# Performance work log

Hardware: AMD Instinct MI355X
Metric: run time of the kernel (lower is better)

Reference implementation:

```python
import jax, jax.numpy as jnp
import numpy as np

B, LATENT, HIDDEN, HEAD_H, OUT = 262144, 64, 512, 64, 4
EPS = 1e-5


def _layernorm(a, g, b):
    mu = jnp.mean(a, axis=-1, keepdims=True)
    var = jnp.mean(jnp.square(a - mu), axis=-1, keepdims=True)
    return (a - mu) / jnp.sqrt(var + EPS) * g + b


def _leaky(a):
    return jnp.where(a >= 0, a, 0.2 * a)


def setup_inputs() -> dict:
    key = jax.random.key(0)
    ks = jax.random.split(key, 12)
    s = lambda fan_in: 1.0 / np.sqrt(fan_in)
    return {
        "z": jax.random.normal(ks[0], (B, LATENT), dtype=jnp.float32),
        "x": jax.random.randint(ks[1], (B,), 0, 2, dtype=jnp.int32),
        "y": jax.random.randint(ks[2], (B,), 0, 2, dtype=jnp.int32),
        # encoder params (Linear stored as [in, out])
        "W1": jax.random.normal(ks[3], (LATENT, HIDDEN), dtype=jnp.float32) * s(LATENT),
        "b1": jnp.zeros((HIDDEN,), dtype=jnp.float32),
        "g1": jnp.ones((HIDDEN,), dtype=jnp.float32),
        "beta1": jnp.zeros((HIDDEN,), dtype=jnp.float32),
        "W2": jax.random.normal(ks[4], (HIDDEN, HIDDEN), dtype=jnp.float32) * s(HIDDEN),
        "b2": jnp.zeros((HIDDEN,), dtype=jnp.float32),
        "g2": jnp.ones((HIDDEN,), dtype=jnp.float32),
        "beta2": jnp.zeros((HIDDEN,), dtype=jnp.float32),
        # 4 setting-specific heads, stacked on leading axis k = 2*x + y
        "Wh1": jax.random.normal(ks[5], (4, HIDDEN, HEAD_H), dtype=jnp.float32) * s(HIDDEN),
        "bh1": jnp.zeros((4, HEAD_H), dtype=jnp.float32),
        "Wh2": jax.random.normal(ks[6], (4, HEAD_H, OUT), dtype=jnp.float32) * s(HEAD_H),
        "bh2": jnp.zeros((4, OUT), dtype=jnp.float32),
    }


def reference(z, x, y, W1, b1, g1, beta1, W2, b2, g2, beta2, Wh1, bh1, Wh2, bh2):
    # encoder: Linear -> LayerNorm -> LeakyReLU(0.2), twice
    h = _leaky(_layernorm(z @ W1 + b1, g1, beta1))          # [B, HIDDEN]
    h = _leaky(_layernorm(h @ W2 + b2, g2, beta2))          # [B, HIDDEN]
    # all 4 heads in one pass, then per-row select (equivalent to mask routing)
    t = jax.nn.relu(jnp.einsum("bh,khd->bkd", h, Wh1) + bh1)  # [B, 4, HEAD_H]
    logits_all = jnp.einsum("bkd,kdo->bko", t, Wh2) + bh2     # [B, 4, OUT]
    k = 2 * x + y                                              # head index per row
    logits = logits_all[jnp.arange(logits_all.shape[0]), k]    # [B, OUT]
    return jax.nn.softmax(logits, axis=-1)
```

## Files before the change

kernel.cpp:

```cpp
#include <hip/hip_runtime.h>

#define MT 48
#define TS 520
#define NROWS 262144
#define EPSV 1e-5f

typedef __attribute__((ext_vector_type(8))) short short8;
typedef __attribute__((ext_vector_type(4))) float floatx4;
typedef __attribute__((ext_vector_type(2))) float floatx2;
typedef __attribute__((ext_vector_type(4))) unsigned int uintx4;
typedef __attribute__((ext_vector_type(2))) unsigned int uintx2;

__device__ __forceinline__ unsigned short f2bf(float f) {
    unsigned u = __builtin_bit_cast(unsigned, f);
    u += 0x7fff + ((u >> 16) & 1);
    return (unsigned short)(u >> 16);
}
__device__ __forceinline__ float bf2f(short s) {
    unsigned u = ((unsigned)(unsigned short)s) << 16;
    return __builtin_bit_cast(float, u);
}
__device__ __forceinline__ unsigned cvtpk(float a, float b) {
    unsigned r;
    asm("v_cvt_pk_bf16_f32 %0, %1, %2" : "=v"(r) : "v"(a), "v"(b));
    return r;
}
template<int C>
__device__ __forceinline__ float dpp_add(float v) {
    int t = __builtin_amdgcn_update_dpp(0, __builtin_bit_cast(int, v), C, 0xf, 0xf, true);
    return v + __builtin_bit_cast(float, t);
}
__device__ __forceinline__ float red16(float v) {
    v = dpp_add<0x111>(v);
    v = dpp_add<0x112>(v);
    v = dpp_add<0x114>(v);
    v = dpp_add<0x118>(v);
    return v;
}

__global__ void convert_weights(const float* __restrict__ W1, const float* __restrict__ W2,
                                const float* __restrict__ Wh1, short* __restrict__ ws) {
    int idx = blockIdx.x * 256 + threadIdx.x;
    if (idx < 32768) {
        int j = idx & 7, lane = (idx >> 3) & 63, c = idx >> 9;
        int ks = c & 1, nt = (c >> 1) & 7, w = c >> 4;
        int k = ks * 32 + (lane >> 4) * 8 + j;
        int n = w * 128 + nt * 16 + (lane & 15);
        ws[idx] = (short)f2bf(W1[k * 512 + n]);
    } else if (idx < 32768 + 262144) {
        int jdx = idx - 32768;
        int j = jdx & 7, lane = (jdx >> 3) & 63, c = jdx >> 9;
        int nt = c & 7, ks = (c >> 3) & 15, w = c >> 7;
        int kp = ks * 32 + (lane >> 4) * 8 + j;
        int k  = (kp & 0x180) + ((kp & 7) << 4) + ((kp >> 3) & 15);
        int n = w * 128 + nt * 16 + (lane & 15);
        ws[idx] = (short)f2bf(W2[k * 512 + n]);
    } else if (idx < 32768 + 262144 + 131072) {
        int jdx = idx - (32768 + 262144);
        int j = jdx & 7, lane = (jdx >> 3) & 63, c = jdx >> 9;
        int nt = c & 3, ks = (c >> 2) & 15, w = c >> 6;
        int kp = ks * 32 + (lane >> 4) * 8 + j;
        int k  = (kp & 0x180) + ((kp & 7) << 4) + ((kp >> 3) & 15);
        int col = w * 64 + nt * 16 + (lane & 15);
        int kk = col >> 6, d = col & 63;
        ws[idx] = (short)f2bf(Wh1[(kk * 512 + k) * 64 + d]);
    }
}

__global__ __launch_bounds__(256, 2) void fused_kernel(
    const float* __restrict__ z, const int* __restrict__ x, const int* __restrict__ y,
    const float* __restrict__ b1, const float* __restrict__ g1, const float* __restrict__ be1,
    const float* __restrict__ b2, const float* __restrict__ g2, const float* __restrict__ be2,
    const float* __restrict__ bh1, const float* __restrict__ Wh2, const float* __restrict__ bh2,
    const short* __restrict__ ws, float* __restrict__ out)
{
    __shared__ __align__(16) short tile[MT * TS];
    __shared__ float pstats[MT][8];
    __shared__ floatx2 rstats[MT];

    int tid  = threadIdx.x;
    int wave = tid >> 6;
    int lane = tid & 63;
    int quad = lane >> 4;
    int l16  = lane & 15;
    int blk0 = blockIdx.x * MT;
    int nslab = wave * 128;

    const short* bbase1 = ws + wave * (16 * 512) + lane * 8;
    const short* bbase2 = ws + 32768 + wave * (16 * 8 * 512) + lane * 8;
    const short* bbase3 = ws + 32768 + 262144 + wave * (16 * 4 * 512) + lane * 8;

    floatx4 acc[3][8];

#pragma unroll
    for (int mt = 0; mt < 3; mt++)
#pragma unroll
        for (int nt = 0; nt < 8; nt++) acc[mt][nt] = (floatx4){0.f, 0.f, 0.f, 0.f};

    __builtin_amdgcn_s_setprio(1);
#pragma unroll
    for (int ks = 0; ks < 2; ks++) {
        short8 afr[3];
#pragma unroll
        for (int mt = 0; mt < 3; mt++) {
            int row = blk0 + mt * 16 + l16;
            row = (row < NROWS) ? row : (NROWS - 1);
            const float* zp = z + row * 64 + ks * 32 + quad * 8;
            floatx4 f0 = *(const floatx4*)zp;
            floatx4 f1 = *(const floatx4*)(zp + 4);
            uintx4 up;
            up[0] = cvtpk(f0[0], f0[1]); up[1] = cvtpk(f0[2], f0[3]);
            up[2] = cvtpk(f1[0], f1[1]); up[3] = cvtpk(f1[2], f1[3]);
            afr[mt] = __builtin_bit_cast(short8, up);
        }
#pragma unroll
        for (int nt = 0; nt < 8; nt++) {
            short8 b = *(const short8*)(bbase1 + (nt * 2 + ks) * 512);
#pragma unroll
            for (int mt = 0; mt < 3; mt++)
                acc[mt][nt] = __builtin_amdgcn_mfma_f32_16x16x32_bf16(afr[mt], b, acc[mt][nt], 0, 0, 0);
        }
    }
    __builtin_amdgcn_s_setprio(0);

    {
#pragma unroll
        for (int nt = 0; nt < 8; nt++) {
            float bv = b1[nslab + nt * 16 + l16];
#pragma unroll
            for (int mt = 0; mt < 3; mt++)
#pragma unroll
                for (int r2 = 0; r2 < 4; r2++) acc[mt][nt][r2] += bv;
        }
        float sum[3][4] = {}, sq[3][4] = {};
#pragma unroll
        for (int mt = 0; mt < 3; mt++)
#pragma unroll
            for (int nt = 0; nt < 8; nt++)
#pragma unroll
                for (int r2 = 0; r2 < 4; r2++) {
                    float v = acc[mt][nt][r2];
                    sum[mt][r2] += v; sq[mt][r2] += v * v;
                }
#pragma unroll
        for (int mt = 0; mt < 3; mt++)
#pragma unroll
            for (int r2 = 0; r2 < 4; r2++) {
                sum[mt][r2] = red16(sum[mt][r2]);
                sq[mt][r2]  = red16(sq[mt][r2]);
            }
        if (l16 == 15) {
#pragma unroll
            for (int mt = 0; mt < 3; mt++)
#pragma unroll
                for (int r2 = 0; r2 < 4; r2++) {
                    int row = mt * 16 + quad * 4 + r2;
                    *(floatx2*)&pstats[row][wave * 2] = (floatx2){sum[mt][r2], sq[mt][r2]};
                }
        }
    }
    __syncthreads();
    if (tid < MT) {
        float s = pstats[tid][0] + pstats[tid][2] + pstats[tid][4] + pstats[tid][6];
        float q = pstats[tid][1] + pstats[tid][3] + pstats[tid][5] + pstats[tid][7];
        float mean = s * (1.f / 512.f);
        float var  = q * (1.f / 512.f) - mean * mean;
        rstats[tid] = (floatx2){mean, rsqrtf(var + EPSV)};
    }
    __syncthreads();
    {
        floatx2 st[3][4];
#pragma unroll
        for (int mt = 0; mt < 3; mt++)
#pragma unroll
            for (int r2 = 0; r2 < 4; r2++) st[mt][r2] = rstats[mt * 16 + quad * 4 + r2];
        float gv[8], bev[8];
#pragma unroll
        for (int nt = 0; nt < 8; nt++) {
            int col = nslab + nt * 16 + l16;
            gv[nt] = g1[col]; bev[nt] = be1[col];
        }
#pragma unroll
        for (int mt = 0; mt < 3; mt++)
#pragma unroll
            for (int r2 = 0; r2 < 4; r2++) {
                int row = mt * 16 + quad * 4 + r2;
                float mean = st[mt][r2][0], rstd = st[mt][r2][1];
                float f[8];
#pragma unroll
                for (int nt = 0; nt < 8; nt++) {
                    float v = (acc[mt][nt][r2] - mean) * rstd * gv[nt] + bev[nt];
                    f[nt] = fmaxf(v, 0.2f * v);
                }
                uintx4 up;
                up[0] = cvtpk(f[0], f[1]); up[1] = cvtpk(f[2], f[3]);
                up[2] = cvtpk(f[4], f[5]); up[3] = cvtpk(f[6], f[7]);
                *(uintx4*)&tile[row * TS + nslab + l16 * 8] = up;
            }
    }
    __syncthreads();

#pragma unroll
    for (int mt = 0; mt < 3; mt++)
#pragma unroll
        for (int nt = 0; nt < 8; nt++) acc[mt][nt] = (floatx4){0.f, 0.f, 0.f, 0.f};

    __builtin_amdgcn_s_setprio(1);
    for (int ks = 0; ks < 16; ks++) {
        short8 afr[3];
#pragma unroll
        for (int mt = 0; mt < 3; mt++) {
            int row = mt * 16 + l16;
            afr[mt] = *(const short8*)&tile[row * TS + ks * 32 + quad * 8];
        }
#pragma unroll
        for (int nt = 0; nt < 8; nt++) {
            short8 b = *(const short8*)(bbase2 + (ks * 8 + nt) * 512);
#pragma unroll
            for (int mt = 0; mt < 3; mt++)
                acc[mt][nt] = __builtin_amdgcn_mfma_f32_16x16x32_bf16(afr[mt], b, acc[mt][nt], 0, 0, 0);
        }
    }
    __builtin_amdgcn_s_setprio(0);
    {
#pragma unroll
        for (int nt = 0; nt < 8; nt++) {
            float bv = b2[nslab + nt * 16 + l16];
#pragma unroll
            for (int mt = 0; mt < 3; mt++)
#pragma unroll
                for (int r2 = 0; r2 < 4; r2++) acc[mt][nt][r2] += bv;
        }
        float sum[3][4] = {}, sq[3][4] = {};
#pragma unroll
        for (int mt = 0; mt < 3; mt++)
#pragma unroll
            for (int nt = 0; nt < 8; nt++)
#pragma unroll
                for (int r2 = 0; r2 < 4; r2++) {
                    float v = acc[mt][nt][r2];
                    sum[mt][r2] += v; sq[mt][r2] += v * v;
                }
#pragma unroll
        for (int mt = 0; mt < 3; mt++)
#pragma unroll
            for (int r2 = 0; r2 < 4; r2++) {
                sum[mt][r2] = red16(sum[mt][r2]);
                sq[mt][r2]  = red16(sq[mt][r2]);
            }
        if (l16 == 15) {
#pragma unroll
            for (int mt = 0; mt < 3; mt++)
#pragma unroll
                for (int r2 = 0; r2 < 4; r2++) {
                    int row = mt * 16 + quad * 4 + r2;
                    *(floatx2*)&pstats[row][wave * 2] = (floatx2){sum[mt][r2], sq[mt][r2]};
                }
        }
    }
    __syncthreads();
    if (tid < MT) {
        float s = pstats[tid][0] + pstats[tid][2] + pstats[tid][4] + pstats[tid][6];
        float q = pstats[tid][1] + pstats[tid][3] + pstats[tid][5] + pstats[tid][7];
        float mean = s * (1.f / 512.f);
        float var  = q * (1.f / 512.f) - mean * mean;
        rstats[tid] = (floatx2){mean, rsqrtf(var + EPSV)};
    }
    __syncthreads();
    {
        floatx2 st[3][4];
#pragma unroll
        for (int mt = 0; mt < 3; mt++)
#pragma unroll
            for (int r2 = 0; r2 < 4; r2++) st[mt][r2] = rstats[mt * 16 + quad * 4 + r2];
        float gv[8], bev[8];
#pragma unroll
        for (int nt = 0; nt < 8; nt++) {
            int col = nslab + nt * 16 + l16;
            gv[nt] = g2[col]; bev[nt] = be2[col];
        }
#pragma unroll
        for (int mt = 0; mt < 3; mt++)
#pragma unroll
            for (int r2 = 0; r2 < 4; r2++) {
                int row = mt * 16 + quad * 4 + r2;
                float mean = st[mt][r2][0], rstd = st[mt][r2][1];
                float f[8];
#pragma unroll
                for (int nt = 0; nt < 8; nt++) {
                    float v = (acc[mt][nt][r2] - mean) * rstd * gv[nt] + bev[nt];
                    f[nt] = fmaxf(v, 0.2f * v);
                }
                uintx4 up;
                up[0] = cvtpk(f[0], f[1]); up[1] = cvtpk(f[2], f[3]);
                up[2] = cvtpk(f[4], f[5]); up[3] = cvtpk(f[6], f[7]);
                *(uintx4*)&tile[row * TS + nslab + l16 * 8] = up;
            }
    }
    __syncthreads();

#pragma unroll
    for (int mt = 0; mt < 3; mt++)
#pragma unroll
        for (int nt = 0; nt < 4; nt++) acc[mt][nt] = (floatx4){0.f, 0.f, 0.f, 0.f};

    __builtin_amdgcn_s_setprio(1);
    for (int ks = 0; ks < 16; ks++) {
        short8 afr[3];
#pragma unroll
        for (int mt = 0; mt < 3; mt++) {
            int row = mt * 16 + l16;
            afr[mt] = *(const short8*)&tile[row * TS + ks * 32 + quad * 8];
        }
#pragma unroll
        for (int nt = 0; nt < 4; nt++) {
            short8 b = *(const short8*)(bbase3 + (ks * 4 + nt) * 512);
#pragma unroll
            for (int mt = 0; mt < 3; mt++)
                acc[mt][nt] = __builtin_amdgcn_mfma_f32_16x16x32_bf16(afr[mt], b, acc[mt][nt], 0, 0, 0);
        }
    }
    __builtin_amdgcn_s_setprio(0);
    __syncthreads();
    {
        float bh1v[4];
#pragma unroll
        for (int nt = 0; nt < 4; nt++) bh1v[nt] = bh1[wave * 64 + nt * 16 + l16];
#pragma unroll
        for (int mt = 0; mt < 3; mt++)
#pragma unroll
            for (int r2 = 0; r2 < 4; r2++) {
                int row = mt * 16 + quad * 4 + r2;
                float f[4];
#pragma unroll
                for (int nt = 0; nt < 4; nt++) {
                    float v = acc[mt][nt][r2] + bh1v[nt];
                    f[nt] = (v > 0.f) ? v : 0.f;
                }
                uintx2 up = {cvtpk(f[0], f[1]), cvtpk(f[2], f[3])};
                *(uintx2*)&tile[row * TS + wave * 64 + l16 * 4] = up;
            }
    }
    __syncthreads();

    {
        int r = tid >> 2, is = tid & 3;
        if (r < MT) {
            int grow = blk0 + r;
            int gsafe = (grow < NROWS) ? grow : (NROWS - 1);
            int kk = 2 * x[gsafe] + y[gsafe];
            const short* tp = &tile[r * TS + kk * 64 + is * 16];
            short8 ta = *(const short8*)tp;
            short8 tb = *(const short8*)(tp + 8);
            const float* wp = Wh2 + kk * 256;
            float lg0 = 0.f, lg1 = 0.f, lg2 = 0.f, lg3 = 0.f;
#pragma unroll
            for (int e = 0; e < 8; e++) {
                int d0 = (e & 3) * 16 + 4 * is + (e >> 2);
                float t0 = bf2f(ta[e]);
                floatx4 w0 = *(const floatx4*)(wp + d0 * 4);
                float t1 = bf2f(tb[e]);
                floatx4 w1 = *(const floatx4*)(wp + (d0 + 2) * 4);
                lg0 += t0 * w0[0] + t1 * w1[0];
                lg1 += t0 * w0[1] + t1 * w1[1];
                lg2 += t0 * w0[2] + t1 * w1[2];
                lg3 += t0 * w0[3] + t1 * w1[3];
            }
#pragma unroll
            for (int off = 1; off < 4; off <<= 1) {
                lg0 += __shfl_xor(lg0, off, 64);
                lg1 += __shfl_xor(lg1, off, 64);
                lg2 += __shfl_xor(lg2, off, 64);
                lg3 += __shfl_xor(lg3, off, 64);
            }
            if (is == 0 && grow < NROWS) {
                lg0 += bh2[kk * 4 + 0]; lg1 += bh2[kk * 4 + 1];
                lg2 += bh2[kk * 4 + 2]; lg3 += bh2[kk * 4 + 3];
                float m = fmaxf(fmaxf(lg0, lg1), fmaxf(lg2, lg3));
                float e0 = __expf(lg0 - m), e1 = __expf(lg1 - m);
                float e2 = __expf(lg2 - m), e3 = __expf(lg3 - m);
                float inv = 1.f / (e0 + e1 + e2 + e3);
                floatx4 o = {e0 * inv, e1 * inv, e2 * inv, e3 * inv};
                *(floatx4*)(out + grow * 4) = o;
            }
        }
    }
}

extern "C" void kernel_launch(void* const* d_in, const int* in_sizes, int n_in,
                              void* d_out, int out_size, void* d_ws, size_t ws_size,
                              hipStream_t stream) {
    const float* z   = (const float*)d_in[0];
    const int*   x   = (const int*)d_in[1];
    const int*   y   = (const int*)d_in[2];
    const float* W1  = (const float*)d_in[3];
    const float* b1  = (const float*)d_in[4];
    const float* g1  = (const float*)d_in[5];
    const float* be1 = (const float*)d_in[6];
    const float* W2  = (const float*)d_in[7];
    const float* b2  = (const float*)d_in[8];
    const float* g2  = (const float*)d_in[9];
    const float* be2 = (const float*)d_in[10];
    const float* Wh1 = (const float*)d_in[11];
    const float* bh1 = (const float*)d_in[12];
    const float* Wh2 = (const float*)d_in[13];
    const float* bh2 = (const float*)d_in[14];
    short* ws = (short*)d_ws;
    float* out = (float*)d_out;

    hipLaunchKernelGGL(convert_weights, dim3(1664), dim3(256), 0, stream, W1, W2, Wh1, ws);
    hipLaunchKernelGGL(fused_kernel, dim3((NROWS + MT - 1) / MT), dim3(256), 0, stream,
                       z, x, y, b1, g1, be1, b2, g2, be2, bh1, Wh2, bh2,
                       (const short*)ws, out);
}
```

Measured before the change: 401.0 us.

## Double-buffer global weight fragment loads and pack LayerNorm math into paired-float ops

Hidden-layer and head GEMM loops are fully unrolled by two with ping-pong register buffers for B-operand weight fragments. The next k-step's global loads are issued before the current step's MFMAs, and the first fragment is prefetched ahead of the LayerNorm epilogue so weight latency overlaps compute. LayerNorm bias add, statistics and normalize steps now use v_pk_add/mul/fma_f32 on pairs of rows, with the stats shared-memory layout changed to suit. This raises register pressure (16 extra short8 fragments) at launch bounds (256,2), which risks spills or reduced occupancy.

```diff
diff --git a/kernel.cpp b/kernel.cpp
--- a/kernel.cpp
+++ b/kernel.cpp
@@ -24,6 +24,15 @@
     unsigned r;
     asm("v_cvt_pk_bf16_f32 %0, %1, %2" : "=v"(r) : "v"(a), "v"(b));
     return r;
+}
+__device__ __forceinline__ floatx2 pk_add(floatx2 a, floatx2 b) {
+    floatx2 d; asm("v_pk_add_f32 %0, %1, %2" : "=v"(d) : "v"(a), "v"(b)); return d;
+}
+__device__ __forceinline__ floatx2 pk_mul(floatx2 a, floatx2 b) {
+    floatx2 d; asm("v_pk_mul_f32 %0, %1, %2" : "=v"(d) : "v"(a), "v"(b)); return d;
+}
+__device__ __forceinline__ floatx2 pk_fma(floatx2 a, floatx2 b, floatx2 c) {
+    floatx2 d; asm("v_pk_fma_f32 %0, %1, %2, %3" : "=v"(d) : "v"(a), "v"(b), "v"(c)); return d;
 }
 template<int C>
 __device__ __forceinline__ float dpp_add(float v) {
@@ -75,8 +84,10 @@
     const short* __restrict__ ws, float* __restrict__ out)
 {
     __shared__ __align__(16) short tile[MT * TS];
-    __shared__ float pstats[MT][8];
-    __shared__ floatx2 rstats[MT];
+    __shared__ float psum[4][MT];
+    __shared__ float psq[4][MT];
+    __shared__ float rmean[MT];
+    __shared__ float rrstd[MT];
 
     int tid  = threadIdx.x;
     int wave = tid >> 6;
@@ -91,6 +102,8 @@
     const short* bbase3 = ws + 32768 + 262144 + wave * (16 * 4 * 512) + lane * 8;
 
     floatx4 acc[3][8];
+    short8 b2a[8], b2b[8];
+    short8 b3a[4], b3b[4];
 
 #pragma unroll
     for (int mt = 0; mt < 3; mt++)
@@ -123,79 +136,92 @@
     }
     __builtin_amdgcn_s_setprio(0);
 
-    {
+#pragma unroll
+    for (int nt = 0; nt < 8; nt++) b2a[nt] = *(const short8*)(bbase2 + nt * 512);
+
+    {
+        floatx2 s2[3][2] = {}, q2[3][2] = {};
 #pragma unroll
         for (int nt = 0; nt < 8; nt++) {
             float bv = b1[nslab + nt * 16 + l16];
-#pragma unroll
-            for (int mt = 0; mt < 3; mt++)
-#pragma unroll
-                for (int r2 = 0; r2 < 4; r2++) acc[mt][nt][r2] += bv;
-        }
-        float sum[3][4] = {}, sq[3][4] = {};
-#pragma unroll
-        for (int mt = 0; mt < 3; mt++)
-#pragma unroll
-            for (int nt = 0; nt < 8; nt++)
-#pragma unroll
-                for (int r2 = 0; r2 < 4; r2++) {
-                    float v = acc[mt][nt][r2];
-                    sum[mt][r2] += v; sq[mt][r2] += v * v;
+            floatx2 bb = {bv, bv};
+#pragma unroll
+            for (int mt = 0; mt < 3; mt++) {
+                floatx2 v01 = {acc[mt][nt][0], acc[mt][nt][1]};
+                floatx2 v23 = {acc[mt][nt][2], acc[mt][nt][3]};
+                v01 = pk_add(v01, bb); v23 = pk_add(v23, bb);
+                acc[mt][nt][0] = v01[0]; acc[mt][nt][1] = v01[1];
+                acc[mt][nt][2] = v23[0]; acc[mt][nt][3] = v23[1];
+                s2[mt][0] = pk_add(s2[mt][0], v01); q2[mt][0] = pk_fma(v01, v01, q2[mt][0]);
+                s2[mt][1] = pk_add(s2[mt][1], v23); q2[mt][1] = pk_fma(v23, v23, q2[mt][1]);
+            }
+        }
+#pragma unroll
+        for (int mt = 0; mt < 3; mt++)
+#pragma unroll
+            for (int pr = 0; pr < 2; pr++) {
+                s2[mt][pr][0] = red16(s2[mt][pr][0]); s2[mt][pr][1] = red16(s2[mt][pr][1]);
+                q2[mt][pr][0] = red16(q2[mt][pr][0]); q2[mt][pr][1] = red16(q2[mt][pr][1]);
+            }
+        if (l16 == 15) {
+#pragma unroll
+            for (int mt = 0; mt < 3; mt++)
+#pragma unroll
+                for (int pr = 0; pr < 2; pr++) {
+                    int row = mt * 16 + quad * 4 + pr * 2;
+                    *(floatx2*)&psum[wave][row] = s2[mt][pr];
+                    *(floatx2*)&psq[wave][row]  = q2[mt][pr];
                 }
-#pragma unroll
-        for (int mt = 0; mt < 3; mt++)
-#pragma unroll
-            for (int r2 = 0; r2 < 4; r2++) {
-                sum[mt][r2] = red16(sum[mt][r2]);
-                sq[mt][r2]  = red16(sq[mt][r2]);
-            }
-        if (l16 == 15) {
-#pragma unroll
-            for (int mt = 0; mt < 3; mt++)
-#pragma unroll
-                for (int r2 = 0; r2 < 4; r2++) {
-                    int row = mt * 16 + quad * 4 + r2;
-                    *(floatx2*)&pstats[row][wave * 2] = (floatx2){sum[mt][r2], sq[mt][r2]};
-                }
         }
     }
     __syncthreads();
     if (tid < MT) {
-        float s = pstats[tid][0] + pstats[tid][2] + pstats[tid][4] + pstats[tid][6];
-        float q = pstats[tid][1] + pstats[tid][3] + pstats[tid][5] + pstats[tid][7];
+        float s = psum[0][tid] + psum[1][tid] + psum[2][tid] + psum[3][tid];
+        float q = psq[0][tid] + psq[1][tid] + psq[2][tid] + psq[3][tid];
         float mean = s * (1.f / 512.f);
         float var  = q * (1.f / 512.f) - mean * mean;
-        rstats[tid] = (floatx2){mean, rsqrtf(var + EPSV)};
-    }
-    __syncthreads();
-    {
-        floatx2 st[3][4];
-#pragma unroll
-        for (int mt = 0; mt < 3; mt++)
-#pragma unroll
-            for (int r2 = 0; r2 < 4; r2++) st[mt][r2] = rstats[mt * 16 + quad * 4 + r2];
-        float gv[8], bev[8];
+        rmean[tid] = -mean;
+        rrstd[tid] = rsqrtf(var + EPSV);
+    }
+    __syncthreads();
+    {
+        floatx2 nm[3][2], rs[3][2];
+#pragma unroll
+        for (int mt = 0; mt < 3; mt++)
+#pragma unroll
+            for (int pr = 0; pr < 2; pr++) {
+                int row = mt * 16 + quad * 4 + pr * 2;
+                nm[mt][pr] = *(const floatx2*)&rmean[row];
+                rs[mt][pr] = *(const floatx2*)&rrstd[row];
+            }
+        floatx2 ggA[8], bbA[8];
 #pragma unroll
         for (int nt = 0; nt < 8; nt++) {
             int col = nslab + nt * 16 + l16;
-            gv[nt] = g1[col]; bev[nt] = be1[col];
-        }
-#pragma unroll
-        for (int mt = 0; mt < 3; mt++)
-#pragma unroll
-            for (int r2 = 0; r2 < 4; r2++) {
-                int row = mt * 16 + quad * 4 + r2;
-                float mean = st[mt][r2][0], rstd = st[mt][r2][1];
-                float f[8];
+            float g = g1[col], be = be1[col];
+            ggA[nt] = (floatx2){g, g}; bbA[nt] = (floatx2){be, be};
+        }
+#pragma unroll
+        for (int mt = 0; mt < 3; mt++)
+#pragma unroll
+            for (int pr = 0; pr < 2; pr++) {
+                float fa[8], fb[8];
 #pragma unroll
                 for (int nt = 0; nt < 8; nt++) {
-                    float v = (acc[mt][nt][r2] - mean) * rstd * gv[nt] + bev[nt];
-                    f[nt] = fmaxf(v, 0.2f * v);
+                    floatx2 v = {acc[mt][nt][2 * pr], acc[mt][nt][2 * pr + 1]};
+                    floatx2 t = pk_mul(pk_add(v, nm[mt][pr]), rs[mt][pr]);
+                    floatx2 f = pk_fma(t, ggA[nt], bbA[nt]);
+                    fa[nt] = fmaxf(f[0], 0.2f * f[0]);
+                    fb[nt] = fmaxf(f[1], 0.2f * f[1]);
                 }
-                uintx4 up;
-                up[0] = cvtpk(f[0], f[1]); up[1] = cvtpk(f[2], f[3]);
-                up[2] = cvtpk(f[4], f[5]); up[3] = cvtpk(f[6], f[7]);
-                *(uintx4*)&tile[row * TS + nslab + l16 * 8] = up;
+                int row = mt * 16 + quad * 4 + pr * 2;
+                uintx4 ua, ub;
+                ua[0] = cvtpk(fa[0], fa[1]); ua[1] = cvtpk(fa[2], fa[3]);
+                ua[2] = cvtpk(fa[4], fa[5]); ua[3] = cvtpk(fa[6], fa[7]);
+                ub[0] = cvtpk(fb[0], fb[1]); ub[1] = cvtpk(fb[2], fb[3]);
+                ub[2] = cvtpk(fb[4], fb[5]); ub[3] = cvtpk(fb[6], fb[7]);
+                *(uintx4*)&tile[row * TS + nslab + l16 * 8]       = ua;
+                *(uintx4*)&tile[(row + 1) * TS + nslab + l16 * 8] = ub;
             }
     }
     __syncthreads();
@@ -206,95 +232,127 @@
         for (int nt = 0; nt < 8; nt++) acc[mt][nt] = (floatx4){0.f, 0.f, 0.f, 0.f};
 
     __builtin_amdgcn_s_setprio(1);
-    for (int ks = 0; ks < 16; ks++) {
-        short8 afr[3];
-#pragma unroll
-        for (int mt = 0; mt < 3; mt++) {
-            int row = mt * 16 + l16;
-            afr[mt] = *(const short8*)&tile[row * TS + ks * 32 + quad * 8];
-        }
-#pragma unroll
-        for (int nt = 0; nt < 8; nt++) {
-            short8 b = *(const short8*)(bbase2 + (ks * 8 + nt) * 512);
-#pragma unroll
-            for (int mt = 0; mt < 3; mt++)
-                acc[mt][nt] = __builtin_amdgcn_mfma_f32_16x16x32_bf16(afr[mt], b, acc[mt][nt], 0, 0, 0);
+#pragma unroll
+    for (int ks = 0; ks < 16; ks += 2) {
+#pragma unroll
+        for (int nt = 0; nt < 8; nt++)
+            b2b[nt] = *(const short8*)(bbase2 + ((ks + 1) * 8 + nt) * 512);
+        {
+            short8 afr[3];
+#pragma unroll
+            for (int mt = 0; mt < 3; mt++)
+                afr[mt] = *(const short8*)&tile[(mt * 16 + l16) * TS + ks * 32 + quad * 8];
+#pragma unroll
+            for (int nt = 0; nt < 8; nt++)
+#pragma unroll
+                for (int mt = 0; mt < 3; mt++)
+                    acc[mt][nt] = __builtin_amdgcn_mfma_f32_16x16x32_bf16(afr[mt], b2a[nt], acc[mt][nt], 0, 0, 0);
+        }
+        if (ks + 2 < 16) {
+#pragma unroll
+            for (int nt = 0; nt < 8; nt++)
+                b2a[nt] = *(const short8*)(bbase2 + ((ks + 2) * 8 + nt) * 512);
+        }
+        {
+            short8 afr[3];
+#pragma unroll
+            for (int mt = 0; mt < 3; mt++)
+                afr[mt] = *(const short8*)&tile[(mt * 16 + l16) * TS + (ks + 1) * 32 + quad * 8];
+#pragma unroll
+            for (int nt = 0; nt < 8; nt++)
+#pragma unroll
+                for (int mt = 0; mt < 3; mt++)
+                    acc[mt][nt] = __builtin_amdgcn_mfma_f32_16x16x32_bf16(afr[mt], b2b[nt], acc[mt][nt], 0, 0, 0);
         }
     }
     __builtin_amdgcn_s_setprio(0);
-    {
+
+#pragma unroll
+    for (int nt = 0; nt < 4; nt++) b3a[nt] = *(const short8*)(bbase3 + nt * 512);
+
+    {
+        floatx2 s2[3][2] = {}, q2[3][2] = {};
 #pragma unroll
         for (int nt = 0; nt < 8; nt++) {
             float bv = b2[nslab + nt * 16 + l16];
-#pragma unroll
-            for (int mt = 0; mt < 3; mt++)
-#pragma unroll
-                for (int r2 = 0; r2 < 4; r2++) acc[mt][nt][r2] += bv;
-        }
-        float sum[3][4] = {}, sq[3][4] = {};
-#pragma unroll
-        for (int mt = 0; mt < 3; mt++)
-#pragma unroll
-            for (int nt = 0; nt < 8; nt++)
-#pragma unroll
-                for (int r2 = 0; r2 < 4; r2++) {
-                    float v = acc[mt][nt][r2];
-                    sum[mt][r2] += v; sq[mt][r2] += v * v;
+            floatx2 bb = {bv, bv};
+#pragma unroll
+            for (int mt = 0; mt < 3; mt++) {
+                floatx2 v01 = {acc[mt][nt][0], acc[mt][nt][1]};
+                floatx2 v23 = {acc[mt][nt][2], acc[mt][nt][3]};
+                v01 = pk_add(v01, bb); v23 = pk_add(v23, bb);
+                acc[mt][nt][0] = v01[0]; acc[mt][nt][1] = v01[1];
+                acc[mt][nt][2] = v23[0]; acc[mt][nt][3] = v23[1];
+                s2[mt][0] = pk_add(s2[mt][0], v01); q2[mt][0] = pk_fma(v01, v01, q2[mt][0]);
+                s2[mt][1] = pk_add(s2[mt][1], v23); q2[mt][1] = pk_fma(v23, v23, q2[mt][1]);
+            }
+        }
+#pragma unroll
+        for (int mt = 0; mt < 3; mt++)
+#pragma unroll
+            for (int pr = 0; pr < 2; pr++) {
+                s2[mt][pr][0] = red16(s2[mt][pr][0]); s2[mt][pr][1] = red16(s2[mt][pr][1]);
+                q2[mt][pr][0] = red16(q2[mt][pr][0]); q2[mt][pr][1] = red16(q2[mt][pr][1]);
+            }
+        if (l16 == 15) {
+#pragma unroll
+            for (int mt = 0; mt < 3; mt++)
+#pragma unroll
+                for (int pr = 0; pr < 2; pr++) {
+                    int row = mt * 16 + quad * 4 + pr * 2;
+                    *(floatx2*)&psum[wave][row] = s2[mt][pr];
+                    *(floatx2*)&psq[wave][row]  = q2[mt][pr];
                 }
-#pragma unroll
-        for (int mt = 0; mt < 3; mt++)
-#pragma unroll
-            for (int r2 = 0; r2 < 4; r2++) {
-                sum[mt][r2] = red16(sum[mt][r2]);
-                sq[mt][r2]  = red16(sq[mt][r2]);
-            }
-        if (l16 == 15) {
-#pragma unroll
-            for (int mt = 0; mt < 3; mt++)
-#pragma unroll
-                for (int r2 = 0; r2 < 4; r2++) {
-                    int row = mt * 16 + quad * 4 + r2;
-                    *(floatx2*)&pstats[row][wave * 2] = (floatx2){sum[mt][r2], sq[mt][r2]};
-                }
         }
     }
     __syncthreads();
     if (tid < MT) {
-        float s = pstats[tid][0] + pstats[tid][2] + pstats[tid][4] + pstats[tid][6];
-        float q = pstats[tid][1] + pstats[tid][3] + pstats[tid][5] + pstats[tid][7];
+        float s = psum[0][tid] + psum[1][tid] + psum[2][tid] + psum[3][tid];
+        float q = psq[0][tid] + psq[1][tid] + psq[2][tid] + psq[3][tid];
         float mean = s * (1.f / 512.f);
         float var  = q * (1.f / 512.f) - mean * mean;
-        rstats[tid] = (floatx2){mean, rsqrtf(var + EPSV)};
-    }
-    __syncthreads();
-    {
-        floatx2 st[3][4];
-#pragma unroll
-        for (int mt = 0; mt < 3; mt++)
-#pragma unroll
-            for (int r2 = 0; r2 < 4; r2++) st[mt][r2] = rstats[mt * 16 + quad * 4 + r2];
-        float gv[8], bev[8];
+        rmean[tid] = -mean;
+        rrstd[tid] = rsqrtf(var + EPSV);
+    }
+    __syncthreads();
+    {
+        floatx2 nm[3][2], rs[3][2];
+#pragma unroll
+        for (int mt = 0; mt < 3; mt++)
+#pragma unroll
+            for (int pr = 0; pr < 2; pr++) {
+                int row = mt * 16 + quad * 4 + pr * 2;
+                nm[mt][pr] = *(const floatx2*)&rmean[row];
+                rs[mt][pr] = *(const floatx2*)&rrstd[row];
+            }
+        floatx2 ggA[8], bbA[8];
 #pragma unroll
         for (int nt = 0; nt < 8; nt++) {
             int col = nslab + nt * 16 + l16;
-            gv[nt] = g2[col]; bev[nt] = be2[col];
-        }
-#pragma unroll
-        for (int mt = 0; mt < 3; mt++)
-#pragma unroll
-            for (int r2 = 0; r2 < 4; r2++) {
-                int row = mt * 16 + quad * 4 + r2;
-                float mean = st[mt][r2][0], rstd = st[mt][r2][1];
-                float f[8];
+            float g = g2[col], be = be2[col];
+            ggA[nt] = (floatx2){g, g}; bbA[nt] = (floatx2){be, be};
+        }
+#pragma unroll
+        for (int mt = 0; mt < 3; mt++)
+#pragma unroll
+            for (int pr = 0; pr < 2; pr++) {
+                float fa[8], fb[8];
 #pragma unroll
                 for (int nt = 0; nt < 8; nt++) {
-                    float v = (acc[mt][nt][r2] - mean) * rstd * gv[nt] + bev[nt];
-                    f[nt] = fmaxf(v, 0.2f * v);
+                    floatx2 v = {acc[mt][nt][2 * pr], acc[mt][nt][2 * pr + 1]};
+                    floatx2 t = pk_mul(pk_add(v, nm[mt][pr]), rs[mt][pr]);
+                    floatx2 f = pk_fma(t, ggA[nt], bbA[nt]);
+                    fa[nt] = fmaxf(f[0], 0.2f * f[0]);
+                    fb[nt] = fmaxf(f[1], 0.2f * f[1]);
                 }
-                uintx4 up;
-                up[0] = cvtpk(f[0], f[1]); up[1] = cvtpk(f[2], f[3]);
-                up[2] = cvtpk(f[4], f[5]); up[3] = cvtpk(f[6], f[7]);
-                *(uintx4*)&tile[row * TS + nslab + l16 * 8] = up;
+                int row = mt * 16 + quad * 4 + pr * 2;
+                uintx4 ua, ub;
+                ua[0] = cvtpk(fa[0], fa[1]); ua[1] = cvtpk(fa[2], fa[3]);
+                ua[2] = cvtpk(fa[4], fa[5]); ua[3] = cvtpk(fa[6], fa[7]);
+                ub[0] = cvtpk(fb[0], fb[1]); ub[1] = cvtpk(fb[2], fb[3]);
+                ub[2] = cvtpk(fb[4], fb[5]); ub[3] = cvtpk(fb[6], fb[7]);
+                *(uintx4*)&tile[row * TS + nslab + l16 * 8]       = ua;
+                *(uintx4*)&tile[(row + 1) * TS + nslab + l16 * 8] = ub;
             }
     }
     __syncthreads();
@@ -305,19 +363,37 @@
         for (int nt = 0; nt < 4; nt++) acc[mt][nt] = (floatx4){0.f, 0.f, 0.f, 0.f};
 
     __builtin_amdgcn_s_setprio(1);
-    for (int ks = 0; ks < 16; ks++) {
-        short8 afr[3];
-#pragma unroll
-        for (int mt = 0; mt < 3; mt++) {
-            int row = mt * 16 + l16;
-            afr[mt] = *(const short8*)&tile[row * TS + ks * 32 + quad * 8];
-        }
-#pragma unroll
-        for (int nt = 0; nt < 4; nt++) {
-            short8 b = *(const short8*)(bbase3 + (ks * 4 + nt) * 512);
-#pragma unroll
-            for (int mt = 0; mt < 3; mt++)
-                acc[mt][nt] = __builtin_amdgcn_mfma_f32_16x16x32_bf16(afr[mt], b, acc[mt][nt], 0, 0, 0);
+#pragma unroll
+    for (int ks = 0; ks < 16; ks += 2) {
+#pragma unroll
+        for (int nt = 0; nt < 4; nt++)
+            b3b[nt] = *(const short8*)(bbase3 + ((ks + 1) * 4 + nt) * 512);
+        {
+            short8 afr[3];
+#pragma unroll
+            for (int mt = 0; mt < 3; mt++)
+                afr[mt] = *(const short8*)&tile[(mt * 16 + l16) * TS + ks * 32 + quad * 8];
+#pragma unroll
+            for (int nt = 0; nt < 4; nt++)
+#pragma unroll
+                for (int mt = 0; mt < 3; mt++)
+                    acc[mt][nt] = __builtin_amdgcn_mfma_f32_16x16x32_bf16(afr[mt], b3a[nt], acc[mt][nt], 0, 0, 0);
+        }
+        if (ks + 2 < 16) {
+#pragma unroll
+            for (int nt = 0; nt < 4; nt++)
+                b3a[nt] = *(const short8*)(bbase3 + ((ks + 2) * 4 + nt) * 512);
+        }
+        {
+            short8 afr[3];
+#pragma unroll
+            for (int mt = 0; mt < 3; mt++)
+                afr[mt] = *(const short8*)&tile[(mt * 16 + l16) * TS + (ks + 1) * 32 + quad * 8];
+#pragma unroll
+            for (int nt = 0; nt < 4; nt++)
+#pragma unroll
+                for (int mt = 0; mt < 3; mt++)
+                    acc[mt][nt] = __builtin_amdgcn_mfma_f32_16x16x32_bf16(afr[mt], b3b[nt], acc[mt][nt], 0, 0, 0);
         }
     }
     __builtin_amdgcn_s_setprio(0);
```

Measured after the change: 436.3 us. +8.8%, slower.
